# Kernel tuning notes

Hardware: AMD Instinct MI355X
Metric: run time of the kernel (lower is better)

## Reference

```python
import jax, jax.numpy as jnp
import numpy as np

N_NODES = 50000
DEG = 16
N_EDGES = N_NODES * DEG
H = 8
D = 32
NEG_SLOPE = 0.2


def setup_inputs() -> dict:
    key = jax.random.key(0)
    k1, k2, k3, k4 = jax.random.split(key, 4)
    feat = jax.random.normal(k1, (N_NODES, H * D), dtype=jnp.float32)
    attn_l = jax.random.normal(k2, (1, H, D), dtype=jnp.float32) * 0.1
    attn_r = jax.random.normal(k3, (1, H, D), dtype=jnp.float32) * 0.1
    bias = jnp.zeros((H * D,), dtype=jnp.float32)
    # every dst node has in-degree DEG (no zero-in-degree nodes)
    dst = jnp.repeat(jnp.arange(N_NODES, dtype=jnp.int32), DEG)
    src = jax.random.randint(k4, (N_EDGES,), 0, N_NODES, dtype=jnp.int32)
    return {"feat": feat, "attn_l": attn_l, "attn_r": attn_r, "bias": bias,
            "src": src, "dst": dst}


def reference(feat, attn_l, attn_r, bias, src, dst):
    N = feat.shape[0]
    fs = feat.reshape(N, H, D)                      # [N,H,D]
    el = (fs * attn_l).sum(-1)                      # [N,H]
    er = (fs * attn_r).sum(-1)                      # [N,H]
    # per-edge attention logit: u_add_v + leaky_relu
    e = jax.nn.leaky_relu(el[src] + er[dst], negative_slope=NEG_SLOPE)  # [E,H]
    # segmented (per-dst) softmax over incoming edges
    emax = jax.ops.segment_max(e, dst, num_segments=N)  # [N,H]
    ee = jnp.exp(e - emax[dst])                         # [E,H]
    esum = jax.ops.segment_sum(ee, dst, num_segments=N)  # [N,H]
    a = ee / esum[dst]                                  # [E,H]
    # u_mul_e then sum: weighted scatter-aggregate
    msg = fs[src] * a[:, :, None]                       # [E,H,D]
    rst = jax.ops.segment_sum(msg, dst, num_segments=N)  # [N,H,D]
    rst = rst + bias.reshape(1, H, D)
    return rst
```

## Files before the change

kernel.cpp:

```cpp
#include <hip/hip_runtime.h>

#define HEADS 8
#define DIM 32
#define DEGREE 16
#define NEG_SLOPE 0.2f

__device__ __forceinline__ unsigned short f2bf(float f) {
  unsigned u = __float_as_uint(f);
  unsigned r = (u + 0x7fffu + ((u >> 16) & 1u)) >> 16;
  return (unsigned short)r;
}

template <bool WRITE_BF16>
__global__ __launch_bounds__(256) void elr_kernel(
    const float4* __restrict__ feat4,
    const float4* __restrict__ attn_l4,
    const float4* __restrict__ attn_r4,
    float* __restrict__ el8, float* __restrict__ er8,
    ushort4* __restrict__ featbH, int total4, int N) {
  int t = blockIdx.x * 256 + threadIdx.x;
  if (t >= total4) return;
  float4 v = feat4[t];
  int c4 = t & 63;
  float4 al = attn_l4[c4];
  float4 ar = attn_r4[c4];
  float pl = v.x * al.x + v.y * al.y + v.z * al.z + v.w * al.w;
  float pr = v.x * ar.x + v.y * ar.y + v.z * ar.z + v.w * ar.w;
#pragma unroll
  for (int off = 4; off >= 1; off >>= 1) {
    pl += __shfl_xor(pl, off);
    pr += __shfl_xor(pr, off);
  }
  if ((t & 7) == 0) {
    el8[t >> 3] = pl;
    er8[t >> 3] = pr;
  }
  if (WRITE_BF16) {
    ushort4 b;
    b.x = f2bf(v.x); b.y = f2bf(v.y); b.z = f2bf(v.z); b.w = f2bf(v.w);
    int n = t >> 6, h = c4 >> 3, d4 = c4 & 7;
    featbH[((size_t)h * N + n) * 8 + d4] = b;
  }
}

__global__ __launch_bounds__(256) void weights_kernel(
    const float4* __restrict__ el84,
    const float4* __restrict__ er84,
    const int* __restrict__ srcIdx,
    float* __restrict__ wH, int N) {
  int t = threadIdx.x;
  int n0 = blockIdx.x * 16;
  int nl = t >> 4;
  int n = n0 + nl;
  if (n >= N) return;
  int s = srcIdx[n0 * DEGREE + t];
  float4 e0 = el84[(size_t)s * 2], e1 = el84[(size_t)s * 2 + 1];
  float4 r0 = er84[(size_t)n * 2], r1 = er84[(size_t)n * 2 + 1];
  float l[HEADS] = {e0.x + r0.x, e0.y + r0.y, e0.z + r0.z, e0.w + r0.w,
                    e1.x + r1.x, e1.y + r1.y, e1.z + r1.z, e1.w + r1.w};
  float w[HEADS];
#pragma unroll
  for (int h = 0; h < HEADS; h++) {
    float e = l[h];
    e = e > 0.0f ? e : NEG_SLOPE * e;
    float m = e;
#pragma unroll
    for (int off = 8; off >= 1; off >>= 1) m = fmaxf(m, __shfl_xor(m, off));
    float x = __expf(e - m);
    float ssum = x;
#pragma unroll
    for (int off = 8; off >= 1; off >>= 1) ssum += __shfl_xor(ssum, off);
    w[h] = x / ssum;
  }
#pragma unroll
  for (int h = 0; h < HEADS; h++)
    wH[(size_t)h * N * DEGREE + n0 * DEGREE + t] = w[h];
}

__global__ __launch_bounds__(256) void gat_kernel(
    const uint4* __restrict__ featbH4,
    const float* __restrict__ wH,
    const int* __restrict__ srcIdx,
    const float* __restrict__ bias,
    float* __restrict__ out, int N) {
  int h = blockIdx.x & 7;
  int chunk = blockIdx.x >> 3;
  int t = threadIdx.x;
  int n0 = chunk * 16;
  int n = n0 + (t >> 4);
  if (n >= N) return;
  int sidx = srcIdx[n0 * DEGREE + t];
  float w = wH[(size_t)h * N * DEGREE + n0 * DEGREE + t];

  int lane = t & 63;
  int q = (lane >> 2) & 3;
  int c = lane & 3;
  int base = lane & 48;
  float acc[8];
#pragma unroll
  for (int k = 0; k < 8; k++) acc[k] = 0.0f;
#pragma unroll
  for (int p = 0; p < 4; p++) {
    int j = p * 4 + q;
    int sj = __shfl(sidx, base + j);
    float wj = __shfl(w, base + j);
    uint4 r = featbH4[((size_t)h * N + sj) * 4 + c];
    acc[0] += wj * __uint_as_float(r.x << 16);
    acc[1] += wj * __uint_as_float(r.x & 0xffff0000u);
    acc[2] += wj * __uint_as_float(r.y << 16);
    acc[3] += wj * __uint_as_float(r.y & 0xffff0000u);
    acc[4] += wj * __uint_as_float(r.z << 16);
    acc[5] += wj * __uint_as_float(r.z & 0xffff0000u);
    acc[6] += wj * __uint_as_float(r.w << 16);
    acc[7] += wj * __uint_as_float(r.w & 0xffff0000u);
  }
#pragma unroll
  for (int k = 0; k < 8; k++) {
    acc[k] += __shfl_xor(acc[k], 4);
    acc[k] += __shfl_xor(acc[k], 8);
  }
  if (q == 0) {
    const float4* bias4 = (const float4*)bias;
    int bidx = h * 8 + c * 2;
    float4 b0 = bias4[bidx], b1 = bias4[bidx + 1];
    float4 o0 = make_float4(acc[0] + b0.x, acc[1] + b0.y,
                            acc[2] + b0.z, acc[3] + b0.w);
    float4 o1 = make_float4(acc[4] + b1.x, acc[5] + b1.y,
                            acc[6] + b1.z, acc[7] + b1.w);
    size_t o = (size_t)n * 64 + h * 8 + c * 2;
    ((float4*)out)[o] = o0;
    ((float4*)out)[o + 1] = o1;
  }
}

__global__ __launch_bounds__(256) void gat_fused_kernel(
    const uint4* __restrict__ featbH4,
    const float* __restrict__ el8,
    const float* __restrict__ er8,
    const int* __restrict__ srcIdx,
    const float* __restrict__ bias,
    float* __restrict__ out, int N) {
  int h = blockIdx.x & 7;
  int chunk = blockIdx.x >> 3;
  int t = threadIdx.x;
  int n0 = chunk * 16;
  int n = n0 + (t >> 4);
  if (n >= N) return;
  int sidx = srcIdx[n0 * DEGREE + t];
  float e = el8[(size_t)sidx * 8 + h] + er8[(size_t)n * 8 + h];
  e = e > 0.0f ? e : NEG_SLOPE * e;
  float m = e;
#pragma unroll
  for (int off = 8; off >= 1; off >>= 1) m = fmaxf(m, __shfl_xor(m, off));
  float x = __expf(e - m);
  float ssum = x;
#pragma unroll
  for (int off = 8; off >= 1; off >>= 1) ssum += __shfl_xor(ssum, off);
  float w = x / ssum;

  int lane = t & 63;
  int q = (lane >> 2) & 3;
  int c = lane & 3;
  int base = lane & 48;
  float acc[8];
#pragma unroll
  for (int k = 0; k < 8; k++) acc[k] = 0.0f;
#pragma unroll
  for (int p = 0; p < 4; p++) {
    int j = p * 4 + q;
    int sj = __shfl(sidx, base + j);
    float wj = __shfl(w, base + j);
    uint4 r = featbH4[((size_t)h * N + sj) * 4 + c];
    acc[0] += wj * __uint_as_float(r.x << 16);
    acc[1] += wj * __uint_as_float(r.x & 0xffff0000u);
    acc[2] += wj * __uint_as_float(r.y << 16);
    acc[3] += wj * __uint_as_float(r.y & 0xffff0000u);
    acc[4] += wj * __uint_as_float(r.z << 16);
    acc[5] += wj * __uint_as_float(r.z & 0xffff0000u);
    acc[6] += wj * __uint_as_float(r.w << 16);
    acc[7] += wj * __uint_as_float(r.w & 0xffff0000u);
  }
#pragma unroll
  for (int k = 0; k < 8; k++) {
    acc[k] += __shfl_xor(acc[k], 4);
    acc[k] += __shfl_xor(acc[k], 8);
  }
  if (q == 0) {
    const float4* bias4 = (const float4*)bias;
    int bidx = h * 8 + c * 2;
    float4 b0 = bias4[bidx], b1 = bias4[bidx + 1];
    float4 o0 = make_float4(acc[0] + b0.x, acc[1] + b0.y,
                            acc[2] + b0.z, acc[3] + b0.w);
    float4 o1 = make_float4(acc[4] + b1.x, acc[5] + b1.y,
                            acc[6] + b1.z, acc[7] + b1.w);
    size_t o = (size_t)n * 64 + h * 8 + c * 2;
    ((float4*)out)[o] = o0;
    ((float4*)out)[o + 1] = o1;
  }
}

extern "C" void kernel_launch(void* const* d_in, const int* in_sizes, int n_in,
                              void* d_out, int out_size, void* d_ws, size_t ws_size,
                              hipStream_t stream) {
  const float* feat   = (const float*)d_in[0];
  const float* attn_l = (const float*)d_in[1];
  const float* attn_r = (const float*)d_in[2];
  const float* bias   = (const float*)d_in[3];
  const int*   src    = (const int*)d_in[4];
  float* out = (float*)d_out;

  int total = in_sizes[0];
  int N = total / (HEADS * DIM);
  int total4 = total / 4;
  int nchunks = (N + 15) / 16;

  float* el8 = (float*)d_ws;
  float* er8 = el8 + (size_t)N * HEADS;
  ushort4* featbH = (ushort4*)(er8 + (size_t)N * HEADS);
  float* wH = (float*)(featbH + (size_t)total / 4);

  size_t need_base = (size_t)N * HEADS * 2 * sizeof(float);
  size_t need_feat = need_base + (size_t)total * 2;
  size_t need_full = need_feat + (size_t)N * DEGREE * HEADS * sizeof(float);

  if (ws_size >= need_full) {
    elr_kernel<true><<<(total4 + 255) / 256, 256, 0, stream>>>(
        (const float4*)feat, (const float4*)attn_l, (const float4*)attn_r,
        el8, er8, featbH, total4, N);
    weights_kernel<<<nchunks, 256, 0, stream>>>(
        (const float4*)el8, (const float4*)er8, src, wH, N);
    gat_kernel<<<nchunks * 8, 256, 0, stream>>>(
        (const uint4*)featbH, wH, src, bias, out, N);
  } else {
    elr_kernel<true><<<(total4 + 255) / 256, 256, 0, stream>>>(
        (const float4*)feat, (const float4*)attn_l, (const float4*)attn_r,
        el8, er8, featbH, total4, N);
    gat_fused_kernel<<<nchunks * 8, 256, 0, stream>>>(
        (const uint4*)featbH, el8, er8, src, bias, out, N);
  }
}
```

Before: 162.7 us.

## Switch gathered features and weights to fp16 with packed half2 FMA accumulation

Stores the feature copy and the per-edge softmax weights as fp16 instead of bf16/fp32, halving the bytes written and read for the weights. The aggregation kernel is restructured so each thread owns one node's 8-dim slice and loops over all 16 edges. It loads source indices and weights as vectors and accumulates with packed half2 FMAs, removing the cross-lane shuffles and reductions. The cost is accuracy: accumulating in fp16 and the narrower fp16 exponent range may raise error relative to the fp32 reference.

```diff
diff --git a/kernel.cpp b/kernel.cpp
--- a/kernel.cpp
+++ b/kernel.cpp
@@ -1,17 +1,12 @@
 #include <hip/hip_runtime.h>
+#include <hip/hip_fp16.h>
 
 #define HEADS 8
 #define DIM 32
 #define DEGREE 16
 #define NEG_SLOPE 0.2f
 
-__device__ __forceinline__ unsigned short f2bf(float f) {
-  unsigned u = __float_as_uint(f);
-  unsigned r = (u + 0x7fffu + ((u >> 16) & 1u)) >> 16;
-  return (unsigned short)r;
-}
-
-template <bool WRITE_BF16>
+template <bool WRITE_F16>
 __global__ __launch_bounds__(256) void elr_kernel(
     const float4* __restrict__ feat4,
     const float4* __restrict__ attn_l4,
@@ -35,9 +30,12 @@
     el8[t >> 3] = pl;
     er8[t >> 3] = pr;
   }
-  if (WRITE_BF16) {
+  if (WRITE_F16) {
     ushort4 b;
-    b.x = f2bf(v.x); b.y = f2bf(v.y); b.z = f2bf(v.z); b.w = f2bf(v.w);
+    b.x = __half_as_ushort(__float2half_rn(v.x));
+    b.y = __half_as_ushort(__float2half_rn(v.y));
+    b.z = __half_as_ushort(__float2half_rn(v.z));
+    b.w = __half_as_ushort(__float2half_rn(v.w));
     int n = t >> 6, h = c4 >> 3, d4 = c4 & 7;
     featbH[((size_t)h * N + n) * 8 + d4] = b;
   }
@@ -47,7 +45,7 @@
     const float4* __restrict__ el84,
     const float4* __restrict__ er84,
     const int* __restrict__ srcIdx,
-    float* __restrict__ wH, int N) {
+    __half* __restrict__ wHh, int N) {
   int t = threadIdx.x;
   int n0 = blockIdx.x * 16;
   int nl = t >> 4;
@@ -74,63 +72,82 @@
   }
 #pragma unroll
   for (int h = 0; h < HEADS; h++)
-    wH[(size_t)h * N * DEGREE + n0 * DEGREE + t] = w[h];
+    wHh[(size_t)h * N * DEGREE + n0 * DEGREE + t] = __float2half_rn(w[h]);
 }
 
 __global__ __launch_bounds__(256) void gat_kernel(
     const uint4* __restrict__ featbH4,
-    const float* __restrict__ wH,
-    const int* __restrict__ srcIdx,
+    const uint4* __restrict__ wHh4,
+    const int4* __restrict__ src4,
     const float* __restrict__ bias,
     float* __restrict__ out, int N) {
   int h = blockIdx.x & 7;
   int chunk = blockIdx.x >> 3;
   int t = threadIdx.x;
-  int n0 = chunk * 16;
-  int n = n0 + (t >> 4);
+  int nl = t >> 2, c = t & 3;
+  int n = chunk * 64 + nl;
   if (n >= N) return;
-  int sidx = srcIdx[n0 * DEGREE + t];
-  float w = wH[(size_t)h * N * DEGREE + n0 * DEGREE + t];
-
-  int lane = t & 63;
-  int q = (lane >> 2) & 3;
-  int c = lane & 3;
-  int base = lane & 48;
-  float acc[8];
-#pragma unroll
-  for (int k = 0; k < 8; k++) acc[k] = 0.0f;
-#pragma unroll
-  for (int p = 0; p < 4; p++) {
-    int j = p * 4 + q;
-    int sj = __shfl(sidx, base + j);
-    float wj = __shfl(w, base + j);
-    uint4 r = featbH4[((size_t)h * N + sj) * 4 + c];
-    acc[0] += wj * __uint_as_float(r.x << 16);
-    acc[1] += wj * __uint_as_float(r.x & 0xffff0000u);
-    acc[2] += wj * __uint_as_float(r.y << 16);
-    acc[3] += wj * __uint_as_float(r.y & 0xffff0000u);
-    acc[4] += wj * __uint_as_float(r.z << 16);
-    acc[5] += wj * __uint_as_float(r.z & 0xffff0000u);
-    acc[6] += wj * __uint_as_float(r.w << 16);
-    acc[7] += wj * __uint_as_float(r.w & 0xffff0000u);
-  }
-#pragma unroll
-  for (int k = 0; k < 8; k++) {
-    acc[k] += __shfl_xor(acc[k], 4);
-    acc[k] += __shfl_xor(acc[k], 8);
-  }
-  if (q == 0) {
-    const float4* bias4 = (const float4*)bias;
-    int bidx = h * 8 + c * 2;
-    float4 b0 = bias4[bidx], b1 = bias4[bidx + 1];
-    float4 o0 = make_float4(acc[0] + b0.x, acc[1] + b0.y,
-                            acc[2] + b0.z, acc[3] + b0.w);
-    float4 o1 = make_float4(acc[4] + b1.x, acc[5] + b1.y,
-                            acc[6] + b1.z, acc[7] + b1.w);
-    size_t o = (size_t)n * 64 + h * 8 + c * 2;
-    ((float4*)out)[o] = o0;
-    ((float4*)out)[o + 1] = o1;
-  }
+
+  int4 s0 = src4[(size_t)n * 4 + 0];
+  int4 s1 = src4[(size_t)n * 4 + 1];
+  int4 s2 = src4[(size_t)n * 4 + 2];
+  int4 s3 = src4[(size_t)n * 4 + 3];
+  uint4 w0 = wHh4[((size_t)h * N + n) * 2 + 0];
+  uint4 w1 = wHh4[((size_t)h * N + n) * 2 + 1];
+
+  const __half2 z = __float2half2_rn(0.0f);
+  __half2 a0 = z, a1 = z, a2 = z, a3 = z;
+  __half2 b0 = z, b1 = z, b2 = z, b3 = z;
+
+  size_t hbase = (size_t)h * N;
+
+#define GAT_EDGE(sv, wu, hi, A0, A1, A2, A3)                                 \
+  do {                                                                       \
+    uint4 r = featbH4[(hbase + (unsigned)(sv)) * 4 + c];                     \
+    unsigned short wb = (unsigned short)((hi) ? ((wu) >> 16) : ((wu) & 0xffffu)); \
+    __half2 wj = __half2half2(__ushort_as_half(wb));                         \
+    A0 = __hfma2(wj, *(const __half2*)&r.x, A0);                             \
+    A1 = __hfma2(wj, *(const __half2*)&r.y, A1);                             \
+    A2 = __hfma2(wj, *(const __half2*)&r.z, A2);                             \
+    A3 = __hfma2(wj, *(const __half2*)&r.w, A3);                             \
+  } while (0)
+
+#pragma unroll
+  for (int dummy = 0; dummy < 1; dummy++) {
+    GAT_EDGE(s0.x, w0.x, 0, a0, a1, a2, a3);
+    GAT_EDGE(s0.y, w0.x, 1, a0, a1, a2, a3);
+    GAT_EDGE(s0.z, w0.y, 0, a0, a1, a2, a3);
+    GAT_EDGE(s0.w, w0.y, 1, a0, a1, a2, a3);
+    GAT_EDGE(s1.x, w0.z, 0, a0, a1, a2, a3);
+    GAT_EDGE(s1.y, w0.z, 1, a0, a1, a2, a3);
+    GAT_EDGE(s1.z, w0.w, 0, a0, a1, a2, a3);
+    GAT_EDGE(s1.w, w0.w, 1, a0, a1, a2, a3);
+    GAT_EDGE(s2.x, w1.x, 0, b0, b1, b2, b3);
+    GAT_EDGE(s2.y, w1.x, 1, b0, b1, b2, b3);
+    GAT_EDGE(s2.z, w1.y, 0, b0, b1, b2, b3);
+    GAT_EDGE(s2.w, w1.y, 1, b0, b1, b2, b3);
+    GAT_EDGE(s3.x, w1.z, 0, b0, b1, b2, b3);
+    GAT_EDGE(s3.y, w1.z, 1, b0, b1, b2, b3);
+    GAT_EDGE(s3.z, w1.w, 0, b0, b1, b2, b3);
+    GAT_EDGE(s3.w, w1.w, 1, b0, b1, b2, b3);
+  }
+#undef GAT_EDGE
+
+  float2 f0 = __half22float2(a0), g0 = __half22float2(b0);
+  float2 f1 = __half22float2(a1), g1 = __half22float2(b1);
+  float2 f2 = __half22float2(a2), g2 = __half22float2(b2);
+  float2 f3 = __half22float2(a3), g3 = __half22float2(b3);
+
+  const float4* bias4 = (const float4*)bias;
+  int bidx = h * 8 + c * 2;
+  float4 bb0 = bias4[bidx], bb1 = bias4[bidx + 1];
+  float4 o0 = make_float4(f0.x + g0.x + bb0.x, f0.y + g0.y + bb0.y,
+                          f1.x + g1.x + bb0.z, f1.y + g1.y + bb0.w);
+  float4 o1 = make_float4(f2.x + g2.x + bb1.x, f2.y + g2.y + bb1.y,
+                          f3.x + g3.x + bb1.z, f3.y + g3.y + bb1.w);
+  size_t o = (size_t)n * 64 + h * 8 + c * 2;
+  ((float4*)out)[o] = o0;
+  ((float4*)out)[o + 1] = o1;
 }
 
 __global__ __launch_bounds__(256) void gat_fused_kernel(
@@ -171,14 +188,18 @@
     int sj = __shfl(sidx, base + j);
     float wj = __shfl(w, base + j);
     uint4 r = featbH4[((size_t)h * N + sj) * 4 + c];
-    acc[0] += wj * __uint_as_float(r.x << 16);
-    acc[1] += wj * __uint_as_float(r.x & 0xffff0000u);
-    acc[2] += wj * __uint_as_float(r.y << 16);
-    acc[3] += wj * __uint_as_float(r.y & 0xffff0000u);
-    acc[4] += wj * __uint_as_float(r.z << 16);
-    acc[5] += wj * __uint_as_float(r.z & 0xffff0000u);
-    acc[6] += wj * __uint_as_float(r.w << 16);
-    acc[7] += wj * __uint_as_float(r.w & 0xffff0000u);
+    float2 v0 = __half22float2(*(const __half2*)&r.x);
+    float2 v1 = __half22float2(*(const __half2*)&r.y);
+    float2 v2 = __half22float2(*(const __half2*)&r.z);
+    float2 v3 = __half22float2(*(const __half2*)&r.w);
+    acc[0] += wj * v0.x;
+    acc[1] += wj * v0.y;
+    acc[2] += wj * v1.x;
+    acc[3] += wj * v1.y;
+    acc[4] += wj * v2.x;
+    acc[5] += wj * v2.y;
+    acc[6] += wj * v3.x;
+    acc[7] += wj * v3.y;
   }
 #pragma unroll
   for (int k = 0; k < 8; k++) {
@@ -212,30 +233,31 @@
   int total = in_sizes[0];
   int N = total / (HEADS * DIM);
   int total4 = total / 4;
-  int nchunks = (N + 15) / 16;
+  int nchunks16 = (N + 15) / 16;
+  int nchunks64 = (N + 63) / 64;
 
   float* el8 = (float*)d_ws;
   float* er8 = el8 + (size_t)N * HEADS;
   ushort4* featbH = (ushort4*)(er8 + (size_t)N * HEADS);
-  float* wH = (float*)(featbH + (size_t)total / 4);
+  __half* wHh = (__half*)((char*)featbH + (size_t)total * 2);
 
   size_t need_base = (size_t)N * HEADS * 2 * sizeof(float);
   size_t need_feat = need_base + (size_t)total * 2;
-  size_t need_full = need_feat + (size_t)N * DEGREE * HEADS * sizeof(float);
+  size_t need_full = need_feat + (size_t)N * DEGREE * HEADS * sizeof(__half);
 
   if (ws_size >= need_full) {
     elr_kernel<true><<<(total4 + 255) / 256, 256, 0, stream>>>(
         (const float4*)feat, (const float4*)attn_l, (const float4*)attn_r,
         el8, er8, featbH, total4, N);
-    weights_kernel<<<nchunks, 256, 0, stream>>>(
-        (const float4*)el8, (const float4*)er8, src, wH, N);
-    gat_kernel<<<nchunks * 8, 256, 0, stream>>>(
-        (const uint4*)featbH, wH, src, bias, out, N);
+    weights_kernel<<<nchunks16, 256, 0, stream>>>(
+        (const float4*)el8, (const float4*)er8, src, wHh, N);
+    gat_kernel<<<nchunks64 * 8, 256, 0, stream>>>(
+        (const uint4*)featbH, (const uint4*)wHh, (const int4*)src, bias, out, N);
   } else {
     elr_kernel<true><<<(total4 + 255) / 256, 256, 0, stream>>>(
         (const float4*)feat, (const float4*)attn_l, (const float4*)attn_r,
         el8, er8, featbH, total4, N);
-    gat_fused_kernel<<<nchunks * 8, 256, 0, stream>>>(
+    gat_fused_kernel<<<nchunks16 * 8, 256, 0, stream>>>(
         (const uint4*)featbH, el8, er8, src, bias, out, N);
   }
 }
```

After: 161.7 us. Within noise of the previous version (-0.6%).
